# Kernel tuning notes

Hardware: AMD Instinct MI355X
Metric: run time of the kernel (lower is better)

Reference implementation:

```python
import jax, jax.numpy as jnp
import numpy as np

B, S, F, D, H = 2, 512, 4096, 768, 12

def setup_inputs() -> dict:
    key = jax.random.key(0)
    ks = jax.random.split(key, 7)
    up_facts = jax.random.normal(ks[0], (B, S, F), dtype=jnp.float32)
    # LN scale is strictly positive; shift uniform away from zero
    hook_scale = jax.random.uniform(ks[1], (B, S, 1), dtype=jnp.float32) + 0.5
    probs = jax.random.uniform(ks[2], (B, H, S, S), dtype=jnp.float32)
    down_encoder = jax.random.normal(ks[3], (F, D), dtype=jnp.float32) * 0.02
    up_decoder = jax.random.normal(ks[4], (D, F), dtype=jnp.float32) * 0.02
    W_OV = jax.random.normal(ks[5], (H, D, D), dtype=jnp.float32) * 0.02
    connection_mask = jax.random.randint(ks[6], (F, F), 0, 2).astype(jnp.bool_)
    return {
        "up_facts": up_facts,
        "hook_scale": hook_scale,
        "probs": probs,
        "down_encoder": down_encoder,
        "up_decoder": up_decoder,
        "W_OV": W_OV,
        "connection_mask": connection_mask,
    }

def reference(up_facts, hook_scale, probs, down_encoder, up_decoder, W_OV, connection_mask):
    # virtual weights: [H, f_down, f_up] = down_enc [f,d_out] x W_OV [h,d_in,d_out] x up_dec [d_in,g]
    # contract d_out first (cheap), then d_in (big GEMM per head)
    tmp = jnp.einsum('fo,hio->hfi', down_encoder, W_OV)          # [H, F, D]
    virtual_weights = jnp.einsum('hfi,ig->hfg', tmp, up_decoder)  # [H, F, F]
    virtual_weights = virtual_weights * connection_mask[None]     # sparse connection mask
    up_facts_post_ln = up_facts / hook_scale                       # [B, S, F]
    # OV-circuit contributions per head, then attention-pattern reweighting
    contributions_post_ov = jnp.einsum('bqg,hfg->bhqf', up_facts_post_ln, virtual_weights)
    contributions = jnp.einsum('bhqk,bhkf->bqf', probs, contributions_post_ov)
    return contributions
```

## Files before the change

kernel.cpp:

```cpp
#include <hip/hip_runtime.h>

#define B_ 2
#define S_ 512
#define F_ 4096
#define D_ 768
#define H_ 12

typedef __attribute__((ext_vector_type(8))) short bf16x8;
typedef __attribute__((ext_vector_type(4))) float f32x4;
typedef unsigned short u16;
typedef unsigned int u32;
typedef unsigned long long u64;

__device__ inline u16 f2bf(float f) {
  u32 u = __float_as_uint(f);
  u32 r = (u + 0x7fffu + ((u >> 16) & 1u)) >> 16;
  return (u16)r;
}

__device__ inline void gload16(const void* g, void* l) {
  __builtin_amdgcn_global_load_lds((const __attribute__((address_space(1))) void*)g,
                                   (__attribute__((address_space(3))) void*)l, 16, 0, 0);
}

template <typename OutT, bool MASK, bool ACC, int ZDIV, bool TMFAST>
__global__ __launch_bounds__(256) void gemm_bt(
    const u16* __restrict__ A, long sA1, long sA0, int lda,
    const u16* __restrict__ Bm, long sB1, long sB0, int ldb,
    OutT* __restrict__ C, long sC1, long sC0, int ldc,
    int K, const u32* __restrict__ maskbits) {
  constexpr int BK = 64;
  __shared__ u16 sA[128 * BK];
  __shared__ u16 sB[128 * BK];
  const int z = blockIdx.z;
  const int z1 = z / ZDIV, z0 = z % ZDIV;
  A += z1 * sA1 + z0 * sA0;
  Bm += z1 * sB1 + z0 * sB0;
  C += z1 * sC1 + z0 * sC0;
  const int gx = gridDim.x, gy = gridDim.y;
  const int nwg = gx * gy;
  const int lin = blockIdx.y * gx + blockIdx.x;
  const int q8 = nwg >> 3, r8 = nwg & 7;
  const int xcd = lin & 7, idx = lin >> 3;
  const int swz = (xcd < r8 ? xcd * (q8 + 1) : r8 * (q8 + 1) + (xcd - r8) * q8) + idx;
  const int tm = TMFAST ? (swz % gy) : (swz / gx);
  const int tn = TMFAST ? (swz / gy) : (swz % gx);
  const int t = threadIdx.x;
  const int lane = t & 63, wave = t >> 6;
  const int wm = (wave >> 1) * 64, wn = (wave & 1) * 64;
  const int srow = t >> 3;
  const int scol = (((t & 7) ^ (srow & 7))) * 8;
  const u16* Ag = A + (long)(tm * 128 + srow) * lda + scol;
  const u16* Bg = Bm + (long)(tn * 128 + srow) * ldb + scol;
  u16* lA = sA + t * 8;
  u16* lB = sB + t * 8;
  const int lr = lane & 15;
  const int hi = lane >> 4;
  const int x7 = lr & 7;
  f32x4 acc[4][4] = {};
  const int nk = K / BK;
  for (int kt = 0; kt < nk; ++kt) {
    const u16* Agk = Ag + kt * BK;
    const u16* Bgk = Bg + kt * BK;
#pragma unroll
    for (int j = 0; j < 4; ++j) gload16(Agk + (long)j * 32 * lda, lA + j * 2048);
#pragma unroll
    for (int j = 0; j < 4; ++j) gload16(Bgk + (long)j * 32 * ldb, lB + j * 2048);
    __syncthreads();
#pragma unroll
    for (int kk = 0; kk < 2; ++kk) {
      bf16x8 af[4], bfr[4];
#pragma unroll
      for (int mi = 0; mi < 4; ++mi)
        af[mi] = *(const bf16x8*)&sA[(wm + mi * 16 + lr) * BK + (((kk * 4 + hi) ^ x7) << 3)];
#pragma unroll
      for (int ni = 0; ni < 4; ++ni)
        bfr[ni] = *(const bf16x8*)&sB[(wn + ni * 16 + lr) * BK + (((kk * 4 + hi) ^ x7) << 3)];
#pragma unroll
      for (int mi = 0; mi < 4; ++mi)
#pragma unroll
        for (int ni = 0; ni < 4; ++ni)
          acc[mi][ni] = __builtin_amdgcn_mfma_f32_16x16x32_bf16(af[mi], bfr[ni], acc[mi][ni], 0, 0, 0);
    }
    __syncthreads();
  }
  const int r0 = tm * 128 + wm + (hi << 2);
  const int c0 = tn * 128 + wn + lr;
#pragma unroll
  for (int mi = 0; mi < 4; ++mi) {
#pragma unroll
    for (int j = 0; j < 4; ++j) {
      const int row = r0 + mi * 16 + j;
#pragma unroll
      for (int ni = 0; ni < 4; ++ni) {
        const int col = c0 + ni * 16;
        float v = acc[mi][ni][j];
        if (MASK) {
          const int g = col & (F_ - 1);
          const u32 w = maskbits[row * (F_ / 32) + (g >> 5)];
          if (!((w >> (g & 31)) & 1u)) v = 0.0f;
        }
        const long idx = (long)row * ldc + col;
        if constexpr (ACC) {
          C[idx] += v;
        } else if constexpr (sizeof(OutT) == 2) {
          C[idx] = (OutT)f2bf(v);
        } else {
          C[idx] = (OutT)v;
        }
      }
    }
  }
}


__global__ void k_detect_mask(const u32* __restrict__ m, int* flag) {
  const int gid = blockIdx.x * 256 + threadIdx.x;
  const u32 w = m[gid];
  const u64 b = __ballot((w & 0xFFFFFF00u) != 0u);
  if ((threadIdx.x & 63) == 0 && b) atomicOr(flag, 1);
}

__global__ void k_pack_mask(const void* __restrict__ m, u64* __restrict__ bits,
                            const int* __restrict__ flag) {
  const long i = (long)blockIdx.x * 256 + threadIdx.x;
  const int u8mode = *flag;
  const int v = u8mode ? (int)((const unsigned char*)m)[i] : ((const int*)m)[i];
  const u64 b = __ballot(v != 0);
  if ((threadIdx.x & 63) == 0) bits[i >> 6] = b;
}

__global__ void k_cast_bf4(const float* __restrict__ in, u16* __restrict__ out, long n4) {
  const long i = (long)blockIdx.x * 256 + threadIdx.x;
  if (i < n4) {
    const float4 v = ((const float4*)in)[i];
    ushort4 o;
    o.x = f2bf(v.x); o.y = f2bf(v.y); o.z = f2bf(v.z); o.w = f2bf(v.w);
    ((ushort4*)out)[i] = o;
  }
}

__global__ void k_ln_transpose(const float* __restrict__ uf, const float* __restrict__ sc,
                               u16* __restrict__ out) {
  __shared__ float tile[32][33];
  const int b = blockIdx.z;
  const int g0 = blockIdx.x * 32, k0 = blockIdx.y * 32;
  const int x = threadIdx.x, y = threadIdx.y;
#pragma unroll
  for (int i = 0; i < 4; ++i) {
    const int k = k0 + y + i * 8;
    tile[y + i * 8][x] = uf[((long)(b * S_ + k)) * F_ + g0 + x] / sc[b * S_ + k];
  }
  __syncthreads();
#pragma unroll
  for (int i = 0; i < 4; ++i) {
    const int g = g0 + y + i * 8;
    out[((long)(b * F_ + g)) * S_ + k0 + x] = f2bf(tile[x][y + i * 8]);
  }
}

__global__ void k_transpose_cast(const float* __restrict__ in, u16* __restrict__ out, int R, int Cc) {
  __shared__ float tile[32][33];
  const int c0 = blockIdx.x * 32, r0 = blockIdx.y * 32;
  const int x = threadIdx.x, y = threadIdx.y;
#pragma unroll
  for (int i = 0; i < 4; ++i)
    tile[y + i * 8][x] = in[(long)(r0 + y + i * 8) * Cc + c0 + x];
  __syncthreads();
#pragma unroll
  for (int i = 0; i < 4; ++i)
    out[(long)(c0 + y + i * 8) * R + r0 + x] = f2bf(tile[x][y + i * 8]);
}

__global__ void k_reduce_out(const float* __restrict__ part, float* __restrict__ out,
                             long n, int ns) {
  const long i = (long)blockIdx.x * 256 + threadIdx.x;
  const long n4 = n / 4;
  if (i < n4) {
    float4 a = ((const float4*)part)[i];
    for (int s = 1; s < ns; ++s) {
      const float4 b = ((const float4*)part)[i + s * n4];
      a.x += b.x; a.y += b.y; a.z += b.z; a.w += b.w;
    }
    ((float4*)out)[i] = a;
  }
}

extern "C" void kernel_launch(void* const* d_in, const int* in_sizes, int n_in,
                              void* d_out, int out_size, void* d_ws, size_t ws_size,
                              hipStream_t stream) {
  const float* up_facts = (const float*)d_in[0];
  const float* hook_scale = (const float*)d_in[1];
  const float* probs = (const float*)d_in[2];
  const float* down_enc = (const float*)d_in[3];
  const float* up_dec = (const float*)d_in[4];
  const float* w_ov = (const float*)d_in[5];
  const void* cmask = d_in[6];
  float* out = (float*)d_out;

  char* base = (char*)d_ws;
  size_t off = 0;
  auto al = [](size_t b) { return (b + 255) & ~(size_t)255; };
  auto take = [&](size_t bytes) -> char* { char* r = base + off; off += al(bytes); return r; };

  u16* probs_bf = (u16*)take((size_t)B_ * H_ * S_ * S_ * 2);
  u16* upT_post = (u16*)take((size_t)B_ * F_ * S_ * 2);
  u16* dE_bf    = (u16*)take((size_t)F_ * D_ * 2);
  u16* wov_bf   = (u16*)take((size_t)H_ * D_ * D_ * 2);
  u16* upT_dec  = (u16*)take((size_t)F_ * D_ * 2);
  u64* mbits    = (u64*)take((size_t)F_ * F_ / 8);
  int* flag     = (int*)take(256);
  const size_t fixed_end = off;

  int NH = 1;
  for (int cand = 4; cand >= 2; --cand) {
    if (H_ % cand) continue;
    const size_t need = fixed_end + al((size_t)cand * F_ * D_ * 2)
                      + al((size_t)cand * F_ * F_ * 2)
                      + al((size_t)B_ * S_ * cand * F_ * 2)
                      + al((size_t)4 * S_ * F_ * 4);
    if (ws_size >= need) { NH = cand; break; }
  }
  u16* tmp_c  = (u16*)take((size_t)NH * F_ * D_ * 2);
  u16* vw_c   = (u16*)take((size_t)NH * F_ * F_ * 2);
  u16* pup_c  = (u16*)take((size_t)B_ * S_ * NH * F_ * 2);
  float* part = (float*)take((size_t)4 * S_ * F_ * 4);

  hipMemsetAsync(flag, 0, 4, stream);
  k_detect_mask<<<64, 256, 0, stream>>>((const u32*)cmask, flag);
  k_pack_mask<<<(F_ * (long)F_) / 256, 256, 0, stream>>>(cmask, mbits, flag);
  k_cast_bf4<<<((long)B_ * H_ * S_ * S_ / 4 + 255) / 256, 256, 0, stream>>>(
      probs, probs_bf, (long)B_ * H_ * S_ * S_ / 4);
  k_cast_bf4<<<((long)F_ * D_ / 4 + 255) / 256, 256, 0, stream>>>(down_enc, dE_bf, (long)F_ * D_ / 4);
  k_cast_bf4<<<((long)H_ * D_ * D_ / 4 + 255) / 256, 256, 0, stream>>>(w_ov, wov_bf, (long)H_ * D_ * D_ / 4);
  k_ln_transpose<<<dim3(F_ / 32, S_ / 32, B_), dim3(32, 8), 0, stream>>>(up_facts, hook_scale, upT_post);
  k_transpose_cast<<<dim3(F_ / 32, D_ / 32, 1), dim3(32, 8), 0, stream>>>(up_dec, upT_dec, D_, F_);

  const int ldK = NH * F_;
  for (int h0 = 0; h0 < H_; h0 += NH) {
    gemm_bt<u16, false, false, 1, false><<<dim3(D_ / 128, F_ / 128, NH), 256, 0, stream>>>(
        dE_bf, 0, 0, D_,
        wov_bf + (size_t)h0 * D_ * D_, (long)D_ * D_, 0, D_,
        tmp_c, (long)F_ * D_, 0, D_, D_, nullptr);
    gemm_bt<u16, true, false, 1, false><<<dim3(F_ / 128, F_ / 128, NH), 256, 0, stream>>>(
        tmp_c, (long)F_ * D_, 0, D_,
        upT_dec, 0, 0, D_,
        vw_c, (long)F_, 0, ldK, D_, (const u32*)mbits);
    gemm_bt<u16, false, false, 2, false><<<dim3(F_ / 128, S_ / 128, NH * B_), 256, 0, stream>>>(
        probs_bf + (size_t)h0 * S_ * S_, (long)S_ * S_, (long)H_ * S_ * S_, S_,
        upT_post, 0, (long)F_ * S_, S_,
        pup_c, (long)F_, (long)S_ * ldK, ldK, S_, nullptr);
    if (h0 == 0)
      gemm_bt<float, false, false, 2, true><<<dim3(F_ / 128, S_ / 128, 4), 256, 0, stream>>>(
          pup_c, (long)(ldK / 2), (long)S_ * ldK, ldK,
          vw_c, (long)(ldK / 2), 0, ldK,
          part, (long)2 * S_ * F_, (long)S_ * F_, F_, ldK / 2, nullptr);
    else
      gemm_bt<float, false, true, 2, true><<<dim3(F_ / 128, S_ / 128, 4), 256, 0, stream>>>(
          pup_c, (long)(ldK / 2), (long)S_ * ldK, ldK,
          vw_c, (long)(ldK / 2), 0, ldK,
          part, (long)2 * S_ * F_, (long)S_ * F_, F_, ldK / 2, nullptr);
  }
  const long n_out = (long)B_ * S_ * F_;
  k_reduce_out<<<(n_out / 4 + 255) / 256, 256, 0, stream>>>(part, out, n_out, 4);
}
```

Measured before the change: 1.232 ms.

## Add 256x256-tile double-buffered MFMA GEMM for masked virtual-weight product

Adds a dedicated GEMM kernel with 256x256 output tiles, 512 threads, a BK=64 double-buffered LDS pipeline fed by global_load_lds, XCD-aware tile swizzling and nontemporal bf16 stores. It replaces the 128x128 generic kernel for the largest GEMM (virtual weights F x F x D per head, with mask applied in the epilogue). The larger tiles raise arithmetic intensity and cut redundant global reads. In exchange they use more registers and 128KB of LDS per block, which may limit occupancy.

New measurement: 1.308 ms. 6.1% more time.

```diff
diff --git a/kernel.cpp b/kernel.cpp
--- a/kernel.cpp
+++ b/kernel.cpp
@@ -113,6 +113,115 @@
   }
 }
 
+template <bool MASK>
+__global__ __launch_bounds__(512, 2) void gemm_bt256(
+    const u16* __restrict__ A, long sAz, int lda,
+    const u16* __restrict__ Bm, long sBz, int ldb,
+    u16* __restrict__ C, long sCz, int ldc,
+    int K, const u32* __restrict__ maskbits) {
+  constexpr int BK = 64;
+  __shared__ u16 lds[2 * 2 * 256 * BK];
+  const int z = blockIdx.z;
+  A += (long)z * sAz;
+  Bm += (long)z * sBz;
+  C += (long)z * sCz;
+  const int gx = gridDim.x, gy = gridDim.y;
+  const int nwg = gx * gy;
+  const int lin = blockIdx.y * gx + blockIdx.x;
+  const int q8 = nwg >> 3, r8 = nwg & 7;
+  const int xcd = lin & 7, idx = lin >> 3;
+  const int swz = (xcd < r8 ? xcd * (q8 + 1) : r8 * (q8 + 1) + (xcd - r8) * q8) + idx;
+  const int tm = swz / gx, tn = swz % gx;
+  const int t = threadIdx.x;
+  const int lane = t & 63, wave = t >> 6;
+  const int wmr = (wave >> 2) * 128;
+  const int wnr = (wave & 3) * 64;
+  const int srow = t >> 3;
+  const int scol = (((t & 7) ^ (srow & 7))) * 8;
+  const u16* Ag = A + (long)(tm * 256 + srow) * lda + scol;
+  const u16* Bg = Bm + (long)(tn * 256 + srow) * ldb + scol;
+  const int lr = lane & 15;
+  const int hi = lane >> 4;
+  const int x7 = lr & 7;
+  f32x4 acc[8][4] = {};
+  const int nk = K / BK;
+  {
+    u16* lA = lds + t * 8;
+    u16* lB = lds + 16384 + t * 8;
+#pragma unroll
+    for (int j = 0; j < 4; ++j) gload16(Ag + (long)j * 64 * lda, lA + j * 4096);
+#pragma unroll
+    for (int j = 0; j < 4; ++j) gload16(Bg + (long)j * 64 * ldb, lB + j * 4096);
+  }
+  __syncthreads();
+  for (int kt = 0; kt < nk; ++kt) {
+    const int c = kt & 1;
+    const u16* sAc = lds + c * 32768;
+    const u16* sBc = lds + c * 32768 + 16384;
+    if (kt + 1 < nk) {
+      u16* lA = lds + (c ^ 1) * 32768 + t * 8;
+      u16* lB = lds + (c ^ 1) * 32768 + 16384 + t * 8;
+      const u16* Agk = Ag + (kt + 1) * BK;
+      const u16* Bgk = Bg + (kt + 1) * BK;
+#pragma unroll
+      for (int j = 0; j < 4; ++j) gload16(Agk + (long)j * 64 * lda, lA + j * 4096);
+#pragma unroll
+      for (int j = 0; j < 4; ++j) gload16(Bgk + (long)j * 64 * ldb, lB + j * 4096);
+    }
+    bf16x8 bfr[4][2], af[4][2];
+#pragma unroll
+    for (int ni = 0; ni < 4; ++ni)
+#pragma unroll
+      for (int kk = 0; kk < 2; ++kk)
+        bfr[ni][kk] = *(const bf16x8*)&sBc[(wnr + ni * 16 + lr) * BK + (((kk * 4 + hi) ^ x7) << 3)];
+#pragma unroll
+    for (int mi = 0; mi < 4; ++mi)
+#pragma unroll
+      for (int kk = 0; kk < 2; ++kk)
+        af[mi][kk] = *(const bf16x8*)&sAc[(wmr + mi * 16 + lr) * BK + (((kk * 4 + hi) ^ x7) << 3)];
+#pragma unroll
+    for (int kk = 0; kk < 2; ++kk)
+#pragma unroll
+      for (int mi = 0; mi < 4; ++mi)
+#pragma unroll
+        for (int ni = 0; ni < 4; ++ni)
+          acc[mi][ni] = __builtin_amdgcn_mfma_f32_16x16x32_bf16(af[mi][kk], bfr[ni][kk], acc[mi][ni], 0, 0, 0);
+#pragma unroll
+    for (int mi = 0; mi < 4; ++mi)
+#pragma unroll
+      for (int kk = 0; kk < 2; ++kk)
+        af[mi][kk] = *(const bf16x8*)&sAc[(wmr + 64 + mi * 16 + lr) * BK + (((kk * 4 + hi) ^ x7) << 3)];
+#pragma unroll
+    for (int kk = 0; kk < 2; ++kk)
+#pragma unroll
+      for (int mi = 0; mi < 4; ++mi)
+#pragma unroll
+        for (int ni = 0; ni < 4; ++ni)
+          acc[mi + 4][ni] = __builtin_amdgcn_mfma_f32_16x16x32_bf16(af[mi][kk], bfr[ni][kk], acc[mi + 4][ni], 0, 0, 0);
+    __syncthreads();
+  }
+  const int r0 = tm * 256 + wmr + (hi << 2);
+  const int c0 = tn * 256 + wnr + lr;
+#pragma unroll
+  for (int mi = 0; mi < 8; ++mi) {
+#pragma unroll
+    for (int j = 0; j < 4; ++j) {
+      const int row = r0 + mi * 16 + j;
+#pragma unroll
+      for (int ni = 0; ni < 4; ++ni) {
+        const int col = c0 + ni * 16;
+        float v = acc[mi][ni][j];
+        if (MASK) {
+          const int g = col & (F_ - 1);
+          const u32 w = maskbits[row * (F_ / 32) + (g >> 5)];
+          if (!((w >> (g & 31)) & 1u)) v = 0.0f;
+        }
+        __builtin_nontemporal_store((u16)f2bf(v), &C[(long)row * ldc + col]);
+      }
+    }
+  }
+}
+
 
 __global__ void k_detect_mask(const u32* __restrict__ m, int* flag) {
   const int gid = blockIdx.x * 256 + threadIdx.x;
@@ -242,10 +351,10 @@
         dE_bf, 0, 0, D_,
         wov_bf + (size_t)h0 * D_ * D_, (long)D_ * D_, 0, D_,
         tmp_c, (long)F_ * D_, 0, D_, D_, nullptr);
-    gemm_bt<u16, true, false, 1, false><<<dim3(F_ / 128, F_ / 128, NH), 256, 0, stream>>>(
-        tmp_c, (long)F_ * D_, 0, D_,
-        upT_dec, 0, 0, D_,
-        vw_c, (long)F_, 0, ldK, D_, (const u32*)mbits);
+    gemm_bt256<true><<<dim3(F_ / 256, F_ / 256, NH), 512, 0, stream>>>(
+        tmp_c, (long)F_ * D_, D_,
+        upT_dec, 0, D_,
+        vw_c, (long)F_, ldK, D_, (const u32*)mbits);
     gemm_bt<u16, false, false, 2, false><<<dim3(F_ / 128, S_ / 128, NH * B_), 256, 0, stream>>>(
         probs_bf + (size_t)h0 * S_ * S_, (long)S_ * S_, (long)H_ * S_ * S_, S_,
         upT_post, 0, (long)F_ * S_, S_,
```

## Add triple-buffered 256x128 GEMM kernel for virtual-weight and final contraction GEMMs

Applied to the files above, without the earlier changes.

Introduces a new GEMM kernel with 512 threads, 256x128 output tiles, and a three-stage LDS ring fed by async global-to-LDS loads. The next-next K tile is issued before the MFMAs on the current tile run, and setprio raises wave priority during the MFMA block. The two largest GEMMs (masked virtual weights and the final probs-weighted contraction) switch to it. The aim is to hide global load latency and raise reuse per tile, at the cost of one workgroup per CU, about 144KB of LDS, and higher register pressure.

Measured after the change: 1.215 ms. Within noise of the previous version (-1.4%).

```diff
diff --git a/kernel.cpp b/kernel.cpp
--- a/kernel.cpp
+++ b/kernel.cpp
@@ -113,6 +113,114 @@
   }
 }
 
+template <typename OutT, bool MASK, bool ACC, int ZDIV, bool TMFAST>
+__global__ __launch_bounds__(512, 1) void gemm_pipe(
+    const u16* __restrict__ A, long sA1, long sA0, int lda,
+    const u16* __restrict__ Bm, long sB1, long sB0, int ldb,
+    OutT* __restrict__ C, long sC1, long sC0, int ldc,
+    int K, const u32* __restrict__ maskbits) {
+  constexpr int BK = 64;
+  constexpr int BUFW = 24576;
+  __shared__ u16 lds[3 * BUFW];
+  const int z = blockIdx.z;
+  const int z1 = z / ZDIV, z0 = z % ZDIV;
+  A += z1 * sA1 + z0 * sA0;
+  Bm += z1 * sB1 + z0 * sB0;
+  C += z1 * sC1 + z0 * sC0;
+  const int gx = gridDim.x, gy = gridDim.y;
+  const int nwg = gx * gy;
+  const int lin = blockIdx.y * gx + blockIdx.x;
+  const int q8 = nwg >> 3, r8 = nwg & 7;
+  const int xcd = lin & 7, idx = lin >> 3;
+  const int swz = (xcd < r8 ? xcd * (q8 + 1) : r8 * (q8 + 1) + (xcd - r8) * q8) + idx;
+  const int tm = TMFAST ? (swz % gy) : (swz / gx);
+  const int tn = TMFAST ? (swz / gy) : (swz % gx);
+  const int t = threadIdx.x;
+  const int lane = t & 63, wave = t >> 6;
+  const int wm = (wave >> 1) * 64;
+  const int wn = (wave & 1) * 64;
+  const int srow = t >> 3;
+  const int scol = (((t & 7) ^ (srow & 7))) * 8;
+  const u16* Ag = A + (long)(tm * 256 + srow) * lda + scol;
+  const u16* Bg = Bm + (long)(tn * 128 + srow) * ldb + scol;
+  const int lr = lane & 15, hi = lane >> 4, x7 = lr & 7;
+  f32x4 acc[4][4] = {};
+  const int nk = K / BK;
+  auto stage = [&](int kt, int buf) {
+    u16* lA = lds + buf * BUFW + t * 8;
+    u16* lB = lds + buf * BUFW + 16384 + t * 8;
+    const u16* As = Ag + (long)kt * BK;
+    const u16* Bs = Bg + (long)kt * BK;
+#pragma unroll
+    for (int j = 0; j < 4; ++j) gload16(As + (long)j * 64 * lda, lA + j * 4096);
+#pragma unroll
+    for (int j = 0; j < 2; ++j) gload16(Bs + (long)j * 64 * ldb, lB + j * 4096);
+  };
+  stage(0, 0);
+  if (nk > 1) stage(1, 1);
+  int bcur = 0;
+  for (int kt = 0; kt < nk; ++kt) {
+    if (kt + 1 < nk) { asm volatile("s_waitcnt vmcnt(6)" ::: "memory"); }
+    else             { asm volatile("s_waitcnt vmcnt(0)" ::: "memory"); }
+    __builtin_amdgcn_s_barrier();
+    __builtin_amdgcn_sched_barrier(0);
+    if (kt + 2 < nk) {
+      int bst = bcur + 2; if (bst >= 3) bst -= 3;
+      stage(kt + 2, bst);
+    }
+    const u16* sAc = lds + bcur * BUFW;
+    const u16* sBc = lds + bcur * BUFW + 16384;
+    bf16x8 af[4][2], bfr[4][2];
+#pragma unroll
+    for (int mi = 0; mi < 4; ++mi)
+#pragma unroll
+      for (int kk = 0; kk < 2; ++kk)
+        af[mi][kk] = *(const bf16x8*)&sAc[(wm + mi * 16 + lr) * BK + (((kk * 4 + hi) ^ x7) << 3)];
+#pragma unroll
+    for (int ni = 0; ni < 4; ++ni)
+#pragma unroll
+      for (int kk = 0; kk < 2; ++kk)
+        bfr[ni][kk] = *(const bf16x8*)&sBc[(wn + ni * 16 + lr) * BK + (((kk * 4 + hi) ^ x7) << 3)];
+    __builtin_amdgcn_s_setprio(1);
+#pragma unroll
+    for (int kk = 0; kk < 2; ++kk)
+#pragma unroll
+      for (int mi = 0; mi < 4; ++mi)
+#pragma unroll
+        for (int ni = 0; ni < 4; ++ni)
+          acc[mi][ni] = __builtin_amdgcn_mfma_f32_16x16x32_bf16(af[mi][kk], bfr[ni][kk], acc[mi][ni], 0, 0, 0);
+    __builtin_amdgcn_s_setprio(0);
+    bcur += 1; if (bcur >= 3) bcur -= 3;
+  }
+  const int r0 = tm * 256 + wm + (hi << 2);
+  const int c0 = tn * 128 + wn + lr;
+#pragma unroll
+  for (int mi = 0; mi < 4; ++mi) {
+#pragma unroll
+    for (int j = 0; j < 4; ++j) {
+      const int row = r0 + mi * 16 + j;
+#pragma unroll
+      for (int ni = 0; ni < 4; ++ni) {
+        const int col = c0 + ni * 16;
+        float v = acc[mi][ni][j];
+        if (MASK) {
+          const int g = col & (F_ - 1);
+          const u32 w = maskbits[row * (F_ / 32) + (g >> 5)];
+          if (!((w >> (g & 31)) & 1u)) v = 0.0f;
+        }
+        const long cidx = (long)row * ldc + col;
+        if constexpr (ACC) {
+          C[cidx] += v;
+        } else if constexpr (sizeof(OutT) == 2) {
+          C[cidx] = (OutT)f2bf(v);
+        } else {
+          C[cidx] = (OutT)v;
+        }
+      }
+    }
+  }
+}
+
 
 __global__ void k_detect_mask(const u32* __restrict__ m, int* flag) {
   const int gid = blockIdx.x * 256 + threadIdx.x;
@@ -242,7 +350,7 @@
         dE_bf, 0, 0, D_,
         wov_bf + (size_t)h0 * D_ * D_, (long)D_ * D_, 0, D_,
         tmp_c, (long)F_ * D_, 0, D_, D_, nullptr);
-    gemm_bt<u16, true, false, 1, false><<<dim3(F_ / 128, F_ / 128, NH), 256, 0, stream>>>(
+    gemm_pipe<u16, true, false, 1, false><<<dim3(F_ / 128, F_ / 256, NH), 512, 0, stream>>>(
         tmp_c, (long)F_ * D_, 0, D_,
         upT_dec, 0, 0, D_,
         vw_c, (long)F_, 0, ldK, D_, (const u32*)mbits);
@@ -251,12 +359,12 @@
         upT_post, 0, (long)F_ * S_, S_,
         pup_c, (long)F_, (long)S_ * ldK, ldK, S_, nullptr);
     if (h0 == 0)
-      gemm_bt<float, false, false, 2, true><<<dim3(F_ / 128, S_ / 128, 4), 256, 0, stream>>>(
+      gemm_pipe<float, false, false, 2, true><<<dim3(F_ / 128, S_ / 256, 4), 512, 0, stream>>>(
           pup_c, (long)(ldK / 2), (long)S_ * ldK, ldK,
           vw_c, (long)(ldK / 2), 0, ldK,
           part, (long)2 * S_ * F_, (long)S_ * F_, F_, ldK / 2, nullptr);
     else
-      gemm_bt<float, false, true, 2, true><<<dim3(F_ / 128, S_ / 128, 4), 256, 0, stream>>>(
+      gemm_pipe<float, false, true, 2, true><<<dim3(F_ / 128, S_ / 256, 4), 512, 0, stream>>>(
           pup_c, (long)(ldK / 2), (long)S_ * ldK, ldK,
           vw_c, (long)(ldK / 2), 0, ldK,
           part, (long)2 * S_ * F_, (long)S_ * F_, F_, ldK / 2, nullptr);
```
